# Optimization experiments

Measured on AMD Instinct MI355X. Metric: run time of the kernel, lower is better.

The kernel has to match this reference:

```python
import jax, jax.numpy as jnp
import numpy as np

B, N, H, HD = 2, 512, 1024, 512


def setup_inputs() -> dict:
    key = jax.random.key(0)
    ks = jax.random.split(key, 9)
    s = 0.02
    return {
        "emb": jax.random.normal(ks[0], (B, N, H), jnp.float32),
        # start detector: Linear(H->HD), ReLU, Linear(HD->1)
        "W_s1": jax.random.normal(ks[1], (H, HD), jnp.float32) * s,
        "b_s1": jax.random.normal(ks[2], (HD,), jnp.float32) * s,
        "w_s2": jax.random.normal(ks[3], (HD,), jnp.float32) * s,
        "b_s2": jax.random.normal(ks[4], (), jnp.float32) * s,
        # end detector: Linear(2H->HD), ReLU, Linear(HD->1)
        "W_e1": jax.random.normal(ks[5], (2 * H, HD), jnp.float32) * s,
        "b_e1": jax.random.normal(ks[6], (HD,), jnp.float32) * s,
        "w_e2": jax.random.normal(ks[7], (HD,), jnp.float32) * s,
        "b_e2": jax.random.normal(ks[8], (), jnp.float32) * s,
    }


def reference(emb, W_s1, b_s1, w_s2, b_s2, W_e1, b_e1, w_e2, b_e2):
    # start logits: (B, N)
    h_s = jax.nn.relu(jnp.einsum("bnh,hd->bnd", emb, W_s1) + b_s1)
    start_logits = jnp.einsum("bnd,d->bn", h_s, w_s2) + b_s2

    # end logits: math of cat([start_rep, end_rep]) @ W_e1 done as split matmuls
    # (avoids materializing the (B,N,N,2H) concat buffer)
    W1_start, W1_end = W_e1[:H], W_e1[H:]
    a = jnp.einsum("bih,hd->bid", emb, W1_start)  # (B, N, HD) start-token part
    c = jnp.einsum("bjh,hd->bjd", emb, W1_end)    # (B, N, HD) end-token part
    h_e = jax.nn.relu(a[:, :, None, :] + c[:, None, :, :] + b_e1)  # (B, N, N, HD)
    end_logits = jnp.einsum("bijd,d->bij", h_e, w_e2) + b_e2       # (B, N, N)

    return (start_logits, end_logits)
```

## Files before the change

### kernel.cpp

```cpp
#include <hip/hip_runtime.h>
#include <hip/hip_bf16.h>


typedef float f32x4 __attribute__((ext_vector_type(4)));
typedef float f32x2 __attribute__((ext_vector_type(2)));
typedef __bf16 bf16x8 __attribute__((ext_vector_type(8)));

static __device__ __forceinline__ unsigned short f2bf(float f) {
  unsigned int u = __builtin_bit_cast(unsigned int, f);
  u += 0x7FFFu + ((u >> 16) & 1u);
  return (unsigned short)(u >> 16);
}

__global__ __launch_bounds__(256) void prep(
    const float* __restrict__ emb, const float* __restrict__ W_s1,
    const float* __restrict__ W_e1, const float* __restrict__ b_s2,
    const float* __restrict__ b_e2, unsigned short* __restrict__ emb_bf,
    unsigned short* __restrict__ Wt_s, unsigned short* __restrict__ Wt_e,
    float* __restrict__ out) {
  __shared__ float tile[32][33];
  int bx = blockIdx.x, t = threadIdx.x;
  if (bx < 512) {
    int i = bx * 2048 + t * 8;
    f32x4 v0 = *(const f32x4*)&emb[i];
    f32x4 v1 = *(const f32x4*)&emb[i + 4];
    ushort4 o0, o1;
    o0.x = f2bf(v0[0]); o0.y = f2bf(v0[1]);
    o0.z = f2bf(v0[2]); o0.w = f2bf(v0[3]);
    o1.x = f2bf(v1[0]); o1.y = f2bf(v1[1]);
    o1.z = f2bf(v1[2]); o1.w = f2bf(v1[3]);
    *(ushort4*)&emb_bf[i] = o0;
    *(ushort4*)&emb_bf[i + 4] = o1;
  } else if (bx < 2048) {
    const float* in;
    unsigned short* o;
    int R, tid;
    if (bx < 1024) { tid = bx - 512;  in = W_s1; o = Wt_s; R = 1024; }
    else           { tid = bx - 1024; in = W_e1; o = Wt_e; R = 2048; }
    int r0 = (tid >> 4) * 32, c0 = (tid & 15) * 32;
    int a = t >> 3, b4 = t & 7;
    f32x4 v = *(const f32x4*)&in[(size_t)(r0 + a) * 512 + c0 + b4 * 4];
    tile[a][b4 * 4 + 0] = v[0];
    tile[a][b4 * 4 + 1] = v[1];
    tile[a][b4 * 4 + 2] = v[2];
    tile[a][b4 * 4 + 3] = v[3];
    __syncthreads();
    ushort4 o4;
    o4.x = f2bf(tile[b4 * 4 + 0][a]);
    o4.y = f2bf(tile[b4 * 4 + 1][a]);
    o4.z = f2bf(tile[b4 * 4 + 2][a]);
    o4.w = f2bf(tile[b4 * 4 + 3][a]);
    *(ushort4*)&o[(size_t)(c0 + a) * R + r0 + b4 * 4] = o4;
  } else if (bx == 2048) {
    float v = b_s2[0];
    f32x4 o = {v, v, v, v};
    *(f32x4*)&out[t * 4] = o;
  } else {
    float v = b_e2[0];
    f32x4 o = {v, v, v, v};
    *(f32x4*)&out[1024 + (size_t)(bx - 2049) * 1024 + t * 4] = o;
  }
}

__global__ __launch_bounds__(256) void gemm_fused(
    const unsigned short* __restrict__ Aemb,
    const unsigned short* __restrict__ Wt_s,
    const unsigned short* __restrict__ Wt_e,
    const float* __restrict__ b_s1, const float* __restrict__ w_s2,
    const float* __restrict__ b_e1, float* __restrict__ out,
    float* __restrict__ A_mat, float* __restrict__ C_mat) {
  __shared__ unsigned short Al[64][72];
  __shared__ unsigned short Bl[32][72];
  int z = blockIdx.z;
  int n0 = blockIdx.x * 32;
  int m0 = blockIdx.y * 64;
  const unsigned short* Bmat = (z == 0) ? Wt_s : Wt_e;
  int bstride = (z == 0) ? 1024 : 2048;
  int bofs = (z == 2) ? 1024 : 0;

  int t = threadIdx.x, lane = t & 63, wave = t >> 6;
  int wm = wave * 16;
  int lm = lane & 15, g = lane >> 4;

  f32x4 acc[2];
  acc[0] = (f32x4){0.f, 0.f, 0.f, 0.f};
  acc[1] = (f32x4){0.f, 0.f, 0.f, 0.f};

  int ar = t >> 2, ac = (t & 3) * 16;
  int br = t >> 3, bc = (t & 7) * 8;
  for (int k0 = 0; k0 < 1024; k0 += 64) {
    __syncthreads();
    const unsigned short* ap = &Aemb[(size_t)(m0 + ar) * 1024 + k0 + ac];
    *(uint4*)&Al[ar][ac] = *(const uint4*)ap;
    *(uint4*)&Al[ar][ac + 8] = *(const uint4*)(ap + 8);
    *(uint4*)&Bl[br][bc] =
        *(const uint4*)&Bmat[(size_t)(n0 + br) * bstride + bofs + k0 + bc];
    __syncthreads();
#pragma unroll
    for (int kk = 0; kk < 2; ++kk) {
      bf16x8 af = *(const bf16x8*)&Al[wm + lm][kk * 32 + g * 8];
      bf16x8 b0 = *(const bf16x8*)&Bl[lm][kk * 32 + g * 8];
      bf16x8 b1 = *(const bf16x8*)&Bl[16 + lm][kk * 32 + g * 8];
      acc[0] = __builtin_amdgcn_mfma_f32_16x16x32_bf16(af, b0, acc[0], 0, 0, 0);
      acc[1] = __builtin_amdgcn_mfma_f32_16x16x32_bf16(af, b1, acc[1], 0, 0, 0);
    }
  }

  int col0 = n0 + lm, col1 = n0 + 16 + lm;
  if (z == 0) {
    float bs0 = b_s1[col0], bs1 = b_s1[col1];
    float ws0 = w_s2[col0], ws1 = w_s2[col1];
#pragma unroll
    for (int r = 0; r < 4; ++r) {
      float s = fmaxf(acc[0][r] + bs0, 0.f) * ws0 +
                fmaxf(acc[1][r] + bs1, 0.f) * ws1;
      s += __shfl_xor(s, 1);
      s += __shfl_xor(s, 2);
      s += __shfl_xor(s, 4);
      s += __shfl_xor(s, 8);
      if (lm == 0) atomicAdd(&out[m0 + wm + g * 4 + r], s);
    }
  } else {
    float* Out = (z == 1) ? A_mat : C_mat;
    float b0 = (z == 2) ? b_e1[col0] : 0.f;
    float b1 = (z == 2) ? b_e1[col1] : 0.f;
#pragma unroll
    for (int r = 0; r < 4; ++r) {
      int row = m0 + wm + g * 4 + r;
      Out[(size_t)row * 512 + col0] = acc[0][r] + b0;
      Out[(size_t)row * 512 + col1] = acc[1][r] + b1;
    }
  }
}

__global__ __launch_bounds__(256) void pairwise(
    const float* __restrict__ A_mat, const float* __restrict__ C_mat,
    const float* __restrict__ w_e2, float* __restrict__ out) {
  __shared__ f32x2 As_p[32][32];
  __shared__ f32x2 Cs_p[32][64];
  __shared__ f32x2 wlh[128];
  int t = threadIdx.x;
  int b = blockIdx.z >> 1, h = blockIdx.z & 1;
  int j0 = blockIdx.x * 64, i0 = blockIdx.y * 32;
  int dbase = h * 256;

  if (t < 128) wlh[t] = *(const f32x2*)&w_e2[dbase + 2 * t];

  int ti = t & 15, tj = t >> 4;
  f32x2 acc2[2][4];
#pragma unroll
  for (int q = 0; q < 2; ++q)
#pragma unroll
    for (int r = 0; r < 4; ++r) acc2[q][r] = (f32x2){0.f, 0.f};

  const float* Ab = A_mat + (size_t)(b * 512 + i0) * 512 + dbase;
  const float* Cb = C_mat + (size_t)(b * 512 + j0) * 512 + dbase;
  int si = t & 31, sq = t >> 5;
  int sj = t & 63, s2 = t >> 6;
  f32x2 z2 = {0.f, 0.f};

  for (int ch = 0; ch < 4; ++ch) {
    __syncthreads();
    {
      int d0 = sq * 8;
      f32x4 v0 = *(const f32x4*)&Ab[(size_t)si * 512 + ch * 64 + d0];
      f32x4 v1 = *(const f32x4*)&Ab[(size_t)si * 512 + ch * 64 + d0 + 4];
      int dp = d0 >> 1;
      As_p[dp + 0][si] = (f32x2){v0[0], v0[1]};
      As_p[dp + 1][si] = (f32x2){v0[2], v0[3]};
      As_p[dp + 2][si] = (f32x2){v1[0], v1[1]};
      As_p[dp + 3][si] = (f32x2){v1[2], v1[3]};
      int e0 = s2 * 16;
#pragma unroll
      for (int p = 0; p < 4; ++p) {
        f32x4 v = *(const f32x4*)&Cb[(size_t)sj * 512 + ch * 64 + e0 + p * 4];
        int ep = (e0 >> 1) + p * 2;
        Cs_p[ep + 0][sj] = (f32x2){v[0], v[1]};
        Cs_p[ep + 1][sj] = (f32x2){v[2], v[3]};
      }
    }
    __syncthreads();
#pragma unroll 8
    for (int dp = 0; dp < 32; ++dp) {
      f32x2 w2 = wlh[ch * 32 + dp];
      f32x4 av = *(const f32x4*)&As_p[dp][ti * 2];
      f32x4 cv0 = *(const f32x4*)&Cs_p[dp][tj * 4];
      f32x4 cv1 = *(const f32x4*)&Cs_p[dp][tj * 4 + 2];
      f32x2 a0 = {av[0], av[1]}, a1 = {av[2], av[3]};
      f32x2 c0 = {cv0[0], cv0[1]}, c1 = {cv0[2], cv0[3]};
      f32x2 c2 = {cv1[0], cv1[1]}, c3 = {cv1[2], cv1[3]};
      acc2[0][0] += __builtin_elementwise_max(a0 + c0, z2) * w2;
      acc2[0][1] += __builtin_elementwise_max(a0 + c1, z2) * w2;
      acc2[0][2] += __builtin_elementwise_max(a0 + c2, z2) * w2;
      acc2[0][3] += __builtin_elementwise_max(a0 + c3, z2) * w2;
      acc2[1][0] += __builtin_elementwise_max(a1 + c0, z2) * w2;
      acc2[1][1] += __builtin_elementwise_max(a1 + c1, z2) * w2;
      acc2[1][2] += __builtin_elementwise_max(a1 + c2, z2) * w2;
      acc2[1][3] += __builtin_elementwise_max(a1 + c3, z2) * w2;
    }
  }

  float* oe = out + 1024;
#pragma unroll
  for (int q = 0; q < 2; ++q) {
    int i = i0 + ti * 2 + q;
#pragma unroll
    for (int r = 0; r < 4; ++r) {
      float v = acc2[q][r][0] + acc2[q][r][1];
      atomicAdd(&oe[(size_t)(b * 512 + i) * 512 + j0 + tj * 4 + r], v);
    }
  }
}

extern "C" void kernel_launch(void* const* d_in, const int* in_sizes, int n_in,
                              void* d_out, int out_size, void* d_ws,
                              size_t ws_size, hipStream_t stream) {
  const float* emb  = (const float*)d_in[0];
  const float* W_s1 = (const float*)d_in[1];
  const float* b_s1 = (const float*)d_in[2];
  const float* w_s2 = (const float*)d_in[3];
  const float* b_s2 = (const float*)d_in[4];
  const float* W_e1 = (const float*)d_in[5];
  const float* b_e1 = (const float*)d_in[6];
  const float* w_e2 = (const float*)d_in[7];
  const float* b_e2 = (const float*)d_in[8];
  float* out = (float*)d_out;

  char* ws = (char*)d_ws;
  unsigned short* emb_bf = (unsigned short*)(ws);
  unsigned short* Wt_s = (unsigned short*)(ws + 2u * (1u << 20));
  unsigned short* Wt_e = (unsigned short*)(ws + 3u * (1u << 20));
  float* A_mat = (float*)(ws + 5u * (1u << 20));
  float* C_mat = (float*)(ws + 7u * (1u << 20));

  hipLaunchKernelGGL(prep, dim3(2561), dim3(256), 0, stream,
                     emb, W_s1, W_e1, b_s2, b_e2, emb_bf, Wt_s, Wt_e, out);
  hipLaunchKernelGGL(gemm_fused, dim3(16, 16, 3), dim3(256), 0, stream,
                     emb_bf, Wt_s, Wt_e, b_s1, w_s2, b_e1, out, A_mat, C_mat);
  hipLaunchKernelGGL(pairwise, dim3(8, 16, 4), dim3(256), 0, stream,
                     A_mat, C_mat, w_e2, out);
}
```

Measured before the change: 123.2 us.

## Drop D-split and atomics in pairwise kernel, fold end bias into store

The pairwise kernel no longer splits the 512-wide hidden dimension across two blocks. Each block now uses 512 threads and loops over all 8 chunks, so it can write the finished end logits with plain vectorized stores plus b_e2 instead of atomicAdd. The prep kernel therefore stops pre-filling the 2 MB end-logit region with the bias, which removes a full output write pass and the atomic read-modify-write traffic. In exchange, each thread holds a 2x2 tile instead of 2x4, which lowers ILP and register reuse per LDS load, and the grid has half as many blocks.

```diff
diff --git a/kernel.cpp b/kernel.cpp
--- a/kernel.cpp
+++ b/kernel.cpp
@@ -15,9 +15,8 @@
 __global__ __launch_bounds__(256) void prep(
     const float* __restrict__ emb, const float* __restrict__ W_s1,
     const float* __restrict__ W_e1, const float* __restrict__ b_s2,
-    const float* __restrict__ b_e2, unsigned short* __restrict__ emb_bf,
-    unsigned short* __restrict__ Wt_s, unsigned short* __restrict__ Wt_e,
-    float* __restrict__ out) {
+    unsigned short* __restrict__ emb_bf, unsigned short* __restrict__ Wt_s,
+    unsigned short* __restrict__ Wt_e, float* __restrict__ out) {
   __shared__ float tile[32][33];
   int bx = blockIdx.x, t = threadIdx.x;
   if (bx < 512) {
@@ -51,14 +50,10 @@
     o4.z = f2bf(tile[b4 * 4 + 2][a]);
     o4.w = f2bf(tile[b4 * 4 + 3][a]);
     *(ushort4*)&o[(size_t)(c0 + a) * R + r0 + b4 * 4] = o4;
-  } else if (bx == 2048) {
+  } else {
     float v = b_s2[0];
     f32x4 o = {v, v, v, v};
     *(f32x4*)&out[t * 4] = o;
-  } else {
-    float v = b_e2[0];
-    f32x4 o = {v, v, v, v};
-    *(f32x4*)&out[1024 + (size_t)(bx - 2049) * 1024 + t * 4] = o;
   }
 }
 
@@ -133,70 +128,58 @@
   }
 }
 
-__global__ __launch_bounds__(256) void pairwise(
+__global__ __launch_bounds__(512) void pairwise(
     const float* __restrict__ A_mat, const float* __restrict__ C_mat,
-    const float* __restrict__ w_e2, float* __restrict__ out) {
+    const float* __restrict__ w_e2, const float* __restrict__ b_e2,
+    float* __restrict__ out) {
   __shared__ f32x2 As_p[32][32];
   __shared__ f32x2 Cs_p[32][64];
-  __shared__ f32x2 wlh[128];
+  __shared__ f32x2 wl2[256];
   int t = threadIdx.x;
-  int b = blockIdx.z >> 1, h = blockIdx.z & 1;
+  int b = blockIdx.z;
   int j0 = blockIdx.x * 64, i0 = blockIdx.y * 32;
-  int dbase = h * 256;
-
-  if (t < 128) wlh[t] = *(const f32x2*)&w_e2[dbase + 2 * t];
-
-  int ti = t & 15, tj = t >> 4;
-  f32x2 acc2[2][4];
+
+  if (t < 256) wl2[t] = *(const f32x2*)&w_e2[2 * t];
+  float be2 = b_e2[0];
+
+  int ti = t >> 5, tj = t & 31;
+  f32x2 acc2[2][2];
 #pragma unroll
   for (int q = 0; q < 2; ++q)
 #pragma unroll
-    for (int r = 0; r < 4; ++r) acc2[q][r] = (f32x2){0.f, 0.f};
-
-  const float* Ab = A_mat + (size_t)(b * 512 + i0) * 512 + dbase;
-  const float* Cb = C_mat + (size_t)(b * 512 + j0) * 512 + dbase;
+    for (int r = 0; r < 2; ++r) acc2[q][r] = (f32x2){0.f, 0.f};
+
+  const float* Ab = A_mat + (size_t)(b * 512 + i0) * 512;
+  const float* Cb = C_mat + (size_t)(b * 512 + j0) * 512;
   int si = t & 31, sq = t >> 5;
   int sj = t & 63, s2 = t >> 6;
   f32x2 z2 = {0.f, 0.f};
 
-  for (int ch = 0; ch < 4; ++ch) {
+  for (int ch = 0; ch < 8; ++ch) {
     __syncthreads();
     {
-      int d0 = sq * 8;
-      f32x4 v0 = *(const f32x4*)&Ab[(size_t)si * 512 + ch * 64 + d0];
-      f32x4 v1 = *(const f32x4*)&Ab[(size_t)si * 512 + ch * 64 + d0 + 4];
-      int dp = d0 >> 1;
-      As_p[dp + 0][si] = (f32x2){v0[0], v0[1]};
-      As_p[dp + 1][si] = (f32x2){v0[2], v0[3]};
-      As_p[dp + 2][si] = (f32x2){v1[0], v1[1]};
-      As_p[dp + 3][si] = (f32x2){v1[2], v1[3]};
-      int e0 = s2 * 16;
-#pragma unroll
-      for (int p = 0; p < 4; ++p) {
-        f32x4 v = *(const f32x4*)&Cb[(size_t)sj * 512 + ch * 64 + e0 + p * 4];
-        int ep = (e0 >> 1) + p * 2;
-        Cs_p[ep + 0][sj] = (f32x2){v[0], v[1]};
-        Cs_p[ep + 1][sj] = (f32x2){v[2], v[3]};
-      }
+      f32x4 va = *(const f32x4*)&Ab[(size_t)si * 512 + ch * 64 + sq * 4];
+      As_p[sq * 2 + 0][si] = (f32x2){va[0], va[1]};
+      As_p[sq * 2 + 1][si] = (f32x2){va[2], va[3]};
+      f32x4 v0 = *(const f32x4*)&Cb[(size_t)sj * 512 + ch * 64 + s2 * 8];
+      f32x4 v1 = *(const f32x4*)&Cb[(size_t)sj * 512 + ch * 64 + s2 * 8 + 4];
+      Cs_p[s2 * 4 + 0][sj] = (f32x2){v0[0], v0[1]};
+      Cs_p[s2 * 4 + 1][sj] = (f32x2){v0[2], v0[3]};
+      Cs_p[s2 * 4 + 2][sj] = (f32x2){v1[0], v1[1]};
+      Cs_p[s2 * 4 + 3][sj] = (f32x2){v1[2], v1[3]};
     }
     __syncthreads();
 #pragma unroll 8
     for (int dp = 0; dp < 32; ++dp) {
-      f32x2 w2 = wlh[ch * 32 + dp];
+      f32x2 w2 = wl2[ch * 32 + dp];
       f32x4 av = *(const f32x4*)&As_p[dp][ti * 2];
-      f32x4 cv0 = *(const f32x4*)&Cs_p[dp][tj * 4];
-      f32x4 cv1 = *(const f32x4*)&Cs_p[dp][tj * 4 + 2];
+      f32x4 cv = *(const f32x4*)&Cs_p[dp][tj * 2];
       f32x2 a0 = {av[0], av[1]}, a1 = {av[2], av[3]};
-      f32x2 c0 = {cv0[0], cv0[1]}, c1 = {cv0[2], cv0[3]};
-      f32x2 c2 = {cv1[0], cv1[1]}, c3 = {cv1[2], cv1[3]};
+      f32x2 c0 = {cv[0], cv[1]}, c1 = {cv[2], cv[3]};
       acc2[0][0] += __builtin_elementwise_max(a0 + c0, z2) * w2;
       acc2[0][1] += __builtin_elementwise_max(a0 + c1, z2) * w2;
-      acc2[0][2] += __builtin_elementwise_max(a0 + c2, z2) * w2;
-      acc2[0][3] += __builtin_elementwise_max(a0 + c3, z2) * w2;
       acc2[1][0] += __builtin_elementwise_max(a1 + c0, z2) * w2;
       acc2[1][1] += __builtin_elementwise_max(a1 + c1, z2) * w2;
-      acc2[1][2] += __builtin_elementwise_max(a1 + c2, z2) * w2;
-      acc2[1][3] += __builtin_elementwise_max(a1 + c3, z2) * w2;
     }
   }
 
@@ -204,11 +187,10 @@
 #pragma unroll
   for (int q = 0; q < 2; ++q) {
     int i = i0 + ti * 2 + q;
-#pragma unroll
-    for (int r = 0; r < 4; ++r) {
-      float v = acc2[q][r][0] + acc2[q][r][1];
-      atomicAdd(&oe[(size_t)(b * 512 + i) * 512 + j0 + tj * 4 + r], v);
-    }
+    float2 vv;
+    vv.x = acc2[q][0][0] + acc2[q][0][1] + be2;
+    vv.y = acc2[q][1][0] + acc2[q][1][1] + be2;
+    *(float2*)&oe[(size_t)(b * 512 + i) * 512 + j0 + tj * 2] = vv;
   }
 }
 
@@ -233,10 +215,10 @@
   float* A_mat = (float*)(ws + 5u * (1u << 20));
   float* C_mat = (float*)(ws + 7u * (1u << 20));
 
-  hipLaunchKernelGGL(prep, dim3(2561), dim3(256), 0, stream,
-                     emb, W_s1, W_e1, b_s2, b_e2, emb_bf, Wt_s, Wt_e, out);
+  hipLaunchKernelGGL(prep, dim3(2049), dim3(256), 0, stream,
+                     emb, W_s1, W_e1, b_s2, emb_bf, Wt_s, Wt_e, out);
   hipLaunchKernelGGL(gemm_fused, dim3(16, 16, 3), dim3(256), 0, stream,
                      emb_bf, Wt_s, Wt_e, b_s1, w_s2, b_e1, out, A_mat, C_mat);
-  hipLaunchKernelGGL(pairwise, dim3(8, 16, 4), dim3(256), 0, stream,
-                     A_mat, C_mat, w_e2, out);
-}
+  hipLaunchKernelGGL(pairwise, dim3(8, 16, 2), dim3(512), 0, stream,
+                     A_mat, C_mat, w_e2, b_e2, out);
+}
```

Result: faster. 119.0 us, median of 2 (-3.4%).
